# Kernel tuning notes

Measured on AMD Instinct MI355X. Metric: run time of the kernel, lower is better.

The kernel has to match this reference:

```python
import jax, jax.numpy as jnp
import numpy as np


def setup_inputs() -> dict:
    key = jax.random.key(0)
    kx, kw = jax.random.split(key)
    x = jax.random.normal(kx, (32, 112, 112, 128), dtype=jnp.float32)
    stdv = 1.0 / np.sqrt(3 * 3 * 128)
    w = jax.random.normal(kw, (3, 3, 128, 256), dtype=jnp.float32) * stdv
    return {"x": x, "w": w}


def reference(x, w):
    # Binarize weights to {-1, 0, +1} exactly like tf.sign, then standard conv2d.
    binary_w = jnp.sign(w)
    out = jax.lax.conv_general_dilated(
        x, binary_w,
        window_strides=(1, 1),
        padding='SAME',
        dimension_numbers=('NHWC', 'HWIO', 'NHWC'),
    )
    return out
```

## Files before the change

### kernel.cpp

```cpp
#include <hip/hip_runtime.h>
#include <hip/hip_bf16.h>


#define TH 8
#define TW 16
#define PH 10
#define PW 18
#define APIX (PH * PW)
#define ASTRIDE 136

typedef __attribute__((ext_vector_type(8))) short bf16x8;
typedef __attribute__((ext_vector_type(4))) float f32x4;

static __device__ inline ushort f2bf_rne(float f) {
    union { float f; unsigned u; } c; c.f = f;
    unsigned u = c.u;
    unsigned r = (u + 0x7FFFu + ((u >> 16) & 1u)) >> 16;
    return (ushort)r;
}

__global__ void pack_w_kernel(const float* __restrict__ w, ushort* __restrict__ wp) {
    int u = blockIdx.x * 256 + threadIdx.x;
    int n  = u & 127;
    int v  = u >> 7;
    int g  = v & 7;
    int tc = v >> 3;
    int c  = tc % 18;
    int kh = c / 6;
    int r6 = c % 6;
    int kw = r6 >> 1;
    int h  = r6 & 1;
    int t  = tc / 18;
    int icb = h * 64 + g * 8;
    const float* src = w + (size_t)((kh * 3 + kw) * 128 + icb) * 256 + t * 128 + n;
    ushort b[8];
    #pragma unroll
    for (int j = 0; j < 8; ++j) {
        float vv = src[(size_t)j * 256];
        b[j] = (vv > 0.f) ? (ushort)0x3F80u : ((vv < 0.f) ? (ushort)0xBF80u : (ushort)0u);
    }
    int gp = g ^ (n & 7);
    uint4 pv;
    pv.x = (unsigned)b[0] | ((unsigned)b[1] << 16);
    pv.y = (unsigned)b[2] | ((unsigned)b[3] << 16);
    pv.z = (unsigned)b[4] | ((unsigned)b[5] << 16);
    pv.w = (unsigned)b[6] | ((unsigned)b[7] << 16);
    *(uint4*)(wp + ((size_t)(tc * 128 + n) * 8 + gp) * 8) = pv;
}

__global__ __launch_bounds__(256, 2)
void binary_conv_kernel(const float* __restrict__ x, const ushort* __restrict__ wp,
                        float* __restrict__ out)
{
    __shared__ __align__(16) ushort At[APIX * ASTRIDE];
    __shared__ __align__(16) ushort Bt[2 * 128 * 64];

    const int tid = threadIdx.x;
    const int bx  = blockIdx.x;
    const int oc0 = blockIdx.y << 7;
    const int wt   = bx % 7;
    const int ht   = (bx / 7) % 14;
    const int nimg = bx / 98;
    const int h0 = ht * TH;
    const int w0 = wt * TW;

    const ushort* wsrc = wp + (size_t)blockIdx.y * 18 * 8192;
    const int wave = tid >> 6;

    auto issueB = [&](int c, int buf) {
        const ushort* s = wsrc + c * 8192 + tid * 8;
        ushort* l = Bt + buf * 8192 + wave * 512;
        #pragma unroll
        for (int i = 0; i < 4; ++i) {
            __builtin_amdgcn_global_load_lds(
                (const __attribute__((address_space(1))) void*)(s + i * 2048),
                (__attribute__((address_space(3))) void*)(l + i * 2048),
                16, 0, 0);
        }
    };

    issueB(0, 0);

    const float* xbase = x + (size_t)nimg * (112 * 112 * 128);
    for (int g = tid; g < APIX * 32; g += 256) {
        int pix = g >> 5;
        int ic  = (g & 31) << 2;
        int ph  = pix / PW;
        int pw  = pix - ph * PW;
        int hh  = h0 + ph - 1;
        int ww  = w0 + pw - 1;
        uint2 val; val.x = 0u; val.y = 0u;
        if ((unsigned)hh < 112u && (unsigned)ww < 112u) {
            const float4 v = *(const float4*)(xbase + ((size_t)(hh * 112 + ww) * 128 + ic));
            val.x = (unsigned)f2bf_rne(v.x) | ((unsigned)f2bf_rne(v.y) << 16);
            val.y = (unsigned)f2bf_rne(v.z) | ((unsigned)f2bf_rne(v.w) << 16);
        }
        *(uint2*)&At[pix * ASTRIDE + ic] = val;
    }

    const int lane = tid & 63;
    const int wm   = wave >> 1;
    const int wn   = wave & 1;
    const int l15  = lane & 15;
    const int quad = lane >> 4;

    f32x4 acc[4][4];
    #pragma unroll
    for (int mt = 0; mt < 4; ++mt)
        #pragma unroll
        for (int nt = 0; nt < 4; ++nt)
            acc[mt][nt] = (f32x4){0.f, 0.f, 0.f, 0.f};

    __syncthreads();

    for (int c = 0; c < 18; ++c) {
        if (c < 17) issueB(c + 1, (c + 1) & 1);

        const int kh  = c / 6;
        const int r6  = c % 6;
        const int kwv = r6 >> 1;
        const int hlf = r6 & 1;
        const ushort* bbase = Bt + (c & 1) * 8192;

        #pragma unroll
        for (int p = 0; p < 2; ++p) {
            const int ico = hlf * 64 + p * 32 + (quad << 3);
            bf16x8 af[4], bfr[4];
            #pragma unroll
            for (int mt = 0; mt < 4; ++mt) {
                int ph_ = wm * 4 + mt + kh;
                af[mt] = *(const bf16x8*)&At[(ph_ * PW + l15 + kwv) * ASTRIDE + ico];
            }
            #pragma unroll
            for (int nt = 0; nt < 4; ++nt) {
                int nl = wn * 64 + nt * 16 + l15;
                int gph = (p * 4 + quad) ^ (nl & 7);
                bfr[nt] = *(const bf16x8*)&bbase[nl * 64 + gph * 8];
            }
            #pragma unroll
            for (int mt = 0; mt < 4; ++mt)
                #pragma unroll
                for (int nt = 0; nt < 4; ++nt)
                    acc[mt][nt] = __builtin_amdgcn_mfma_f32_16x16x32_bf16(
                        af[mt], bfr[nt], acc[mt][nt], 0, 0, 0);
        }
        __syncthreads();
    }

    float* obase = out + ((size_t)nimg * 112 * 112) * 256 + oc0 + wn * 64 + l15;
    #pragma unroll
    for (int mt = 0; mt < 4; ++mt) {
        #pragma unroll
        for (int r = 0; r < 4; ++r) {
            int m  = wm * 64 + mt * 16 + quad * 4 + r;
            int dh = m >> 4;
            int dw = m & 15;
            float* orow = obase + (size_t)((h0 + dh) * 112 + (w0 + dw)) * 256;
            #pragma unroll
            for (int nt = 0; nt < 4; ++nt)
                orow[nt * 16] = acc[mt][nt][r];
        }
    }
}

extern "C" void kernel_launch(void* const* d_in, const int* in_sizes, int n_in,
                              void* d_out, int out_size, void* d_ws, size_t ws_size,
                              hipStream_t stream) {
    const float* x = (const float*)d_in[0];
    const float* w = (const float*)d_in[1];
    float* out = (float*)d_out;
    ushort* wpack = (ushort*)d_ws;

    hipLaunchKernelGGL(pack_w_kernel, dim3(144), dim3(256), 0, stream, w, wpack);

    dim3 grid(32 * 14 * 7, 2);
    hipLaunchKernelGGL(binary_conv_kernel, grid, dim3(256), 0, stream, x, wpack, out);
}
```

Baseline: 834.1 us.

## Load binarized weights directly into registers, drop LDS B tile and barriers

Repacks the binarized weight buffer into an MFMA-fragment-ordered layout so each lane reads its B fragments straight from global memory into registers. A register double-buffer replaces the LDS staging and the per-chunk __syncthreads. The A tile drops its padded stride in favour of an XOR swizzle, which shrinks LDS use enough to allow 3 blocks per CU. In exchange, register pressure rises from the 16 extra bf16x8 fragments, and each wave fetches weights from global or L2 without sharing them across waves.

```diff
diff --git a/kernel.cpp b/kernel.cpp
--- a/kernel.cpp
+++ b/kernel.cpp
@@ -7,7 +7,6 @@
 #define PH 10
 #define PW 18
 #define APIX (PH * PW)
-#define ASTRIDE 136
 
 typedef __attribute__((ext_vector_type(8))) short bf16x8;
 typedef __attribute__((ext_vector_type(4))) float f32x4;
@@ -21,39 +20,41 @@
 
 __global__ void pack_w_kernel(const float* __restrict__ w, ushort* __restrict__ wp) {
     int u = blockIdx.x * 256 + threadIdx.x;
-    int n  = u & 127;
-    int v  = u >> 7;
-    int g  = v & 7;
-    int tc = v >> 3;
-    int c  = tc % 18;
+    int lane = u & 63;
+    int l15  = lane & 15;
+    int quad = lane >> 4;
+    int v  = u >> 6;
+    int ng = v & 7;
+    int p  = (v >> 3) & 1;
+    int cc = v >> 4;
+    int c  = cc % 18;
+    int t  = cc / 18;
     int kh = c / 6;
     int r6 = c % 6;
     int kw = r6 >> 1;
     int h  = r6 & 1;
-    int t  = tc / 18;
-    int icb = h * 64 + g * 8;
-    const float* src = w + (size_t)((kh * 3 + kw) * 128 + icb) * 256 + t * 128 + n;
+    int oc  = t * 128 + ng * 16 + l15;
+    int icb = h * 64 + (p * 4 + quad) * 8;
+    const float* src = w + (size_t)((kh * 3 + kw) * 128 + icb) * 256 + oc;
     ushort b[8];
     #pragma unroll
     for (int j = 0; j < 8; ++j) {
         float vv = src[(size_t)j * 256];
         b[j] = (vv > 0.f) ? (ushort)0x3F80u : ((vv < 0.f) ? (ushort)0xBF80u : (ushort)0u);
     }
-    int gp = g ^ (n & 7);
     uint4 pv;
     pv.x = (unsigned)b[0] | ((unsigned)b[1] << 16);
     pv.y = (unsigned)b[2] | ((unsigned)b[3] << 16);
     pv.z = (unsigned)b[4] | ((unsigned)b[5] << 16);
     pv.w = (unsigned)b[6] | ((unsigned)b[7] << 16);
-    *(uint4*)(wp + ((size_t)(tc * 128 + n) * 8 + gp) * 8) = pv;
+    *(uint4*)(wp + ((((size_t)cc * 2 + p) * 8 + ng) * 64 + lane) * 8) = pv;
 }
 
-__global__ __launch_bounds__(256, 2)
+__global__ __launch_bounds__(256, 3)
 void binary_conv_kernel(const float* __restrict__ x, const ushort* __restrict__ wp,
                         float* __restrict__ out)
 {
-    __shared__ __align__(16) ushort At[APIX * ASTRIDE];
-    __shared__ __align__(16) ushort Bt[2 * 128 * 64];
+    __shared__ __align__(16) ushort At[APIX * 128];
 
     const int tid = threadIdx.x;
     const int bx  = blockIdx.x;
@@ -64,22 +65,27 @@
     const int h0 = ht * TH;
     const int w0 = wt * TW;
 
-    const ushort* wsrc = wp + (size_t)blockIdx.y * 18 * 8192;
     const int wave = tid >> 6;
+    const int lane = tid & 63;
+    const int l15  = lane & 15;
+    const int quad = lane >> 4;
+    const int wm   = wave >> 1;
+    const int wn   = wave & 1;
 
-    auto issueB = [&](int c, int buf) {
-        const ushort* s = wsrc + c * 8192 + tid * 8;
-        ushort* l = Bt + buf * 8192 + wave * 512;
+    const ushort* wsrc = wp + (size_t)blockIdx.y * 147456
+                            + (size_t)(wn * 4) * 512 + (size_t)lane * 8;
+
+    bf16x8 ba[8], bb[8];
+    auto loadB = [&](bf16x8 (&b)[8], int c) {
+        const ushort* s = wsrc + (size_t)c * 8192;
         #pragma unroll
-        for (int i = 0; i < 4; ++i) {
-            __builtin_amdgcn_global_load_lds(
-                (const __attribute__((address_space(1))) void*)(s + i * 2048),
-                (__attribute__((address_space(3))) void*)(l + i * 2048),
-                16, 0, 0);
-        }
+        for (int p = 0; p < 2; ++p)
+            #pragma unroll
+            for (int nt = 0; nt < 4; ++nt)
+                b[p * 4 + nt] = *(const bf16x8*)(s + (p * 8 + nt) * 512);
     };
 
-    issueB(0, 0);
+    loadB(ba, 0);
 
     const float* xbase = x + (size_t)nimg * (112 * 112 * 128);
     for (int g = tid; g < APIX * 32; g += 256) {
@@ -95,14 +101,9 @@
             val.x = (unsigned)f2bf_rne(v.x) | ((unsigned)f2bf_rne(v.y) << 16);
             val.y = (unsigned)f2bf_rne(v.z) | ((unsigned)f2bf_rne(v.w) << 16);
         }
-        *(uint2*)&At[pix * ASTRIDE + ic] = val;
+        int sw = (((ic >> 3) ^ (pix & 7)) << 3) + (ic & 7);
+        *(uint2*)&At[pix * 128 + sw] = val;
     }
-
-    const int lane = tid & 63;
-    const int wm   = wave >> 1;
-    const int wn   = wave & 1;
-    const int l15  = lane & 15;
-    const int quad = lane >> 4;
 
     f32x4 acc[4][4];
     #pragma unroll
@@ -113,38 +114,35 @@
 
     __syncthreads();
 
-    for (int c = 0; c < 18; ++c) {
-        if (c < 17) issueB(c + 1, (c + 1) & 1);
-
+    auto compute = [&](int c, bf16x8 (&b)[8]) {
         const int kh  = c / 6;
         const int r6  = c % 6;
         const int kwv = r6 >> 1;
         const int hlf = r6 & 1;
-        const ushort* bbase = Bt + (c & 1) * 8192;
-
+        const int col = l15 + kwv;
         #pragma unroll
         for (int p = 0; p < 2; ++p) {
-            const int ico = hlf * 64 + p * 32 + (quad << 3);
-            bf16x8 af[4], bfr[4];
+            const int ch = hlf * 8 + p * 4 + quad;
+            bf16x8 af[4];
             #pragma unroll
             for (int mt = 0; mt < 4; ++mt) {
-                int ph_ = wm * 4 + mt + kh;
-                af[mt] = *(const bf16x8*)&At[(ph_ * PW + l15 + kwv) * ASTRIDE + ico];
-            }
-            #pragma unroll
-            for (int nt = 0; nt < 4; ++nt) {
-                int nl = wn * 64 + nt * 16 + l15;
-                int gph = (p * 4 + quad) ^ (nl & 7);
-                bfr[nt] = *(const bf16x8*)&bbase[nl * 64 + gph * 8];
+                int pix = (wm * 4 + mt + kh) * PW + col;
+                af[mt] = *(const bf16x8*)&At[pix * 128 + ((ch ^ (pix & 7)) << 3)];
             }
             #pragma unroll
             for (int mt = 0; mt < 4; ++mt)
                 #pragma unroll
                 for (int nt = 0; nt < 4; ++nt)
                     acc[mt][nt] = __builtin_amdgcn_mfma_f32_16x16x32_bf16(
-                        af[mt], bfr[nt], acc[mt][nt], 0, 0, 0);
+                        af[mt], b[p * 4 + nt], acc[mt][nt], 0, 0, 0);
         }
-        __syncthreads();
+    };
+
+    for (int cc = 0; cc < 18; cc += 2) {
+        loadB(bb, cc + 1);
+        compute(cc, ba);
+        if (cc + 2 < 18) loadB(ba, cc + 2);
+        compute(cc + 1, bb);
     }
 
     float* obase = out + ((size_t)nimg * 112 * 112) * 256 + oc0 + wn * 64 + l15;
```

New measurement: 747.2 us. 10.4% less time.
